# Kernel optimization log

Hardware: AMD Instinct MI355X
Metric: run time of the kernel (lower is better)

Reference implementation:

```python
import jax, jax.numpy as jnp
import numpy as np

N_NODES = 20000
NUM_STEPS = 6
SIGNS = (1.0, -1.0, 1.0, -1.0, 1.0, -1.0)  # TF_POS, TF_NEG, PPI_POS, PPI_NEG, UNDIR, MIRNA_NEG


def setup_inputs() -> dict:
    key = jax.random.key(0)
    ks = jax.random.split(key, 12)
    B, N, E, H, C = 64, N_NODES, 400000, 64, 32
    return {
        "ctl_base": jax.random.normal(ks[0], (B, N), jnp.float32),
        "u_raw": jax.random.normal(ks[1], (B, N), jnp.float32),
        "cell_idx": jax.random.randint(ks[2], (B,), 0, C, jnp.int32),
        "edge_src": jax.random.randint(ks[3], (6, E), 0, N, jnp.int32),
        "edge_dst": jax.random.randint(ks[4], (6, E), 0, N, jnp.int32),
        "edge_val": jax.random.uniform(ks[5], (6, E), jnp.float32),
        "g_logits": jnp.zeros((6,), jnp.float32),
        "alpha_logits": jnp.zeros((NUM_STEPS,), jnp.float32),
        "cell_emb": jax.random.normal(ks[6], (C, H), jnp.float32),
        "W1": jax.random.normal(ks[7], (3, H), jnp.float32) * 0.1,
        "b1": jnp.zeros((H,), jnp.float32),
        "W2": jax.random.normal(ks[8], (H, 1), jnp.float32) * 0.1,
        "b2": jnp.zeros((1,), jnp.float32),
    }


def _spmm_right(h, src, dst, val):
    # out[b, j] = sum_{e: dst[e]==j} h[b, src[e]] * val[e]   (== h @ A)
    gathered = h.T[src] * val[:, None]  # [E, B]
    return jax.ops.segment_sum(gathered, dst, num_segments=N_NODES).T  # [B, N]


def reference(ctl_base, u_raw, g_logits, alpha_logits, cell_emb,
              W1, b1, W2, b2, edge_val, edge_src, edge_dst, cell_idx):
    g = jax.nn.softplus(g_logits)          # [6] relation gates
    alphas = jax.nn.sigmoid(alpha_logits)  # [num_steps]
    h0 = u_raw
    h = u_raw
    for k in range(NUM_STEPS):
        msg = jnp.zeros_like(h)
        for r in range(6):
            msg = msg + SIGNS[r] * g[r] * _spmm_right(h, edge_src[r], edge_dst[r], edge_val[r])
        a = alphas[k]
        h = a * h0 + (1.0 - a) * msg
    # decode: stack [ctl, u_raw, hK] -> [B, N, 3]
    x = jnp.stack([ctl_base, u_raw, h], axis=-1)
    hd = jax.nn.relu(jnp.einsum('bnf,fh->bnh', x, W1) + b1)  # [B, N, H]
    hd = hd + cell_emb[cell_idx][:, None, :]
    y = (jnp.einsum('bnh,ho->bno', hd, W2) + b2)[..., 0]  # [B, N]
    return y
```

## Files before the change

### kernel.cpp

```cpp
#include <hip/hip_runtime.h>

#define N_NODES 20000
#define HID 64
#define NSTEPS 6
#define NSLICE 8
#define SLICE_SZ (N_NODES / NSLICE)
#define SUBB 64
#define NBLK (NSLICE * SUBB)
#define NB1 512
#define MAGIC 13422

union U16H { unsigned short u; _Float16 h; };
union U4H8 { uint4 u; _Float16 h[8]; };

__device__ __forceinline__ _Float16 us_as_h(unsigned short s) { U16H u; u.u = s; return u.h; }
__device__ __forceinline__ unsigned short h_as_us(_Float16 h) { U16H u; u.h = h; return u.u; }

__device__ __forceinline__ int slice_of(int d) {
    return (int)(((unsigned)d * (unsigned)MAGIC) >> 25);
}
__device__ __forceinline__ float softplusf_(float x) {
    return (x > 0.f) ? (x + log1pf(expf(-x))) : log1pf(expf(x));
}
__device__ __forceinline__ float sigmoidf_(float x) {
    return 1.f / (1.f + expf(-x));
}

__global__ __launch_bounds__(64) void prep_kernel(const float* __restrict__ g_logits,
                                                  const float* __restrict__ alpha_logits,
                                                  const int* __restrict__ cell_idx,
                                                  const float* __restrict__ cell_emb,
                                                  const float* __restrict__ W2,
                                                  const float* __restrict__ b2,
                                                  float* __restrict__ gsign,
                                                  float* __restrict__ alph,
                                                  float* __restrict__ cell_dot) {
    int t = threadIdx.x;
    if (t < 6) gsign[t] = ((t & 1) ? -1.f : 1.f) * softplusf_(g_logits[t]);
    if (t < NSTEPS) alph[t] = sigmoidf_(alpha_logits[t]);
    int ci = cell_idx[t];
    float acc = b2[0];
    for (int hh = 0; hh < HID; ++hh) acc = fmaf(cell_emb[ci * HID + hh], W2[hh], acc);
    cell_dot[t] = acc;
}

__global__ __launch_bounds__(256) void count8_kernel(const int* __restrict__ edst,
                                                     int* __restrict__ gcnt, int TE) {
    __shared__ int lh[8];
    int bk = blockIdx.x;
    int lane = threadIdx.x & 63;
    if (threadIdx.x < 8) lh[threadIdx.x] = 0;
    __syncthreads();
    int chunk = ((TE + NB1 - 1) / NB1 + 255) & ~255;
    int lo = bk * chunk;
    int hi = min(lo + chunk, TE);
    int my = 0;
    for (int ii = 0; ii < chunk; ii += 256) {
        int i = lo + ii + (int)threadIdx.x;
        bool act = i < hi;
        int s = -1;
        if (act) s = slice_of(__builtin_nontemporal_load(edst + i));
#pragma unroll
        for (int q = 0; q < 8; ++q) {
            unsigned long long b = __ballot(s == q);
            if (lane == q) my += (int)__popcll(b);
        }
    }
    if (lane < 8) atomicAdd(&lh[lane], my);
    __syncthreads();
    if (threadIdx.x < 8) gcnt[bk * 8 + threadIdx.x] = lh[threadIdx.x];
}

__global__ __launch_bounds__(256) void scan8_kernel(const int* __restrict__ gcnt,
                                                    int* __restrict__ blkoff,
                                                    int* __restrict__ bbase) {
    __shared__ int psum[8][33];
    int tid = threadIdx.x;
    int s = tid >> 5, g = tid & 31;
    const int per = NB1 / 32;
    int sum = 0;
    for (int b = g * per; b < (g + 1) * per; ++b) sum += gcnt[b * 8 + s];
    psum[s][g] = sum;
    __syncthreads();
    if (tid < 8) {
        int run = 0;
        for (int i = 0; i < 32; ++i) { int v = psum[tid][i]; psum[tid][i] = run; run += v; }
        psum[tid][32] = run;
    }
    __syncthreads();
    int run = psum[s][g];
    for (int b = g * per; b < (g + 1) * per; ++b) {
        blkoff[b * 8 + s] = run;
        run += gcnt[b * 8 + s];
    }
    if (tid == 0) {
        int acc = 0;
        bbase[0] = 0;
        for (int q = 0; q < 8; ++q) { acc += psum[q][32]; bbase[q + 1] = acc; }
    }
}

__global__ __launch_bounds__(256) void bucket_kernel(const int* __restrict__ esrc,
                                                     const int* __restrict__ edst,
                                                     const float* __restrict__ eval,
                                                     const float* __restrict__ gsign,
                                                     const int* __restrict__ blkoff,
                                                     const int* __restrict__ bbase,
                                                     int2* __restrict__ bucket,
                                                     int E, int TE) {
    __shared__ int lcur[8];
    int bk = blockIdx.x;
    int lane = threadIdx.x & 63;
    if (threadIdx.x < 8) lcur[threadIdx.x] = bbase[threadIdx.x] + blkoff[bk * 8 + threadIdx.x];
    __syncthreads();
    int chunk = ((TE + NB1 - 1) / NB1 + 255) & ~255;
    int lo = bk * chunk;
    int hi = min(lo + chunk, TE);
    for (int ii = 0; ii < chunk; ii += 256) {
        int i = lo + ii + (int)threadIdx.x;
        bool act = i < hi;
        int s = -1, meta = 0, cb = 0;
        if (act) {
            int d  = __builtin_nontemporal_load(edst + i);
            int sv = __builtin_nontemporal_load(esrc + i);
            float ev = __builtin_nontemporal_load(eval + i);
            s = slice_of(d);
            int dl = d - s * SLICE_SZ;
            meta = sv | (dl << 16);
            int r = (i >= E) + (i >= 2 * E) + (i >= 3 * E) + (i >= 4 * E) + (i >= 5 * E);
            cb = __float_as_int(gsign[r] * ev);
        }
        int pos = 0;
#pragma unroll
        for (int q = 0; q < 8; ++q) {
            unsigned long long b = __ballot(s == q);
            if (b) {
                int leader = (int)__ffsll(b) - 1;
                int base = 0;
                if (lane == leader) base = atomicAdd(&lcur[q], (int)__popcll(b));
                base = __shfl(base, leader);
                if (s == q) pos = base + (int)__popcll(b & ((1ull << lane) - 1ull));
            }
        }
        if (act) bucket[pos] = make_int2(meta, cb);
    }
}

__global__ __launch_bounds__(256) void hist2db_kernel(const int2* __restrict__ bucket,
                                                      const int* __restrict__ bbase,
                                                      int* __restrict__ blkcnt) {
    __shared__ int lh[SLICE_SZ];
    int bk = blockIdx.x;
    int slice = bk & (NSLICE - 1);
    int sub = bk >> 3;
    for (int b = threadIdx.x; b < SLICE_SZ; b += 256) lh[b] = 0;
    __syncthreads();
    int lo = bbase[slice];
    int total = bbase[slice + 1] - lo;
    int chunk = ((total + SUBB - 1) / SUBB + 255) & ~255;
    int beg = lo + sub * chunk;
    int end = min(beg + chunk, lo + total);
    const int* mp = (const int*)bucket;
    for (int i = beg + (int)threadIdx.x; i < end; i += 256) {
        int meta = __builtin_nontemporal_load(mp + 2 * (size_t)i);
        atomicAdd(&lh[((unsigned)meta) >> 16], 1);
    }
    __syncthreads();
    int* out = blkcnt + (size_t)(slice * SUBB + sub) * SLICE_SZ;
    for (int b = threadIdx.x; b < SLICE_SZ; b += 256) out[b] = lh[b];
}

__global__ __launch_bounds__(256) void colscan_kernel(int* __restrict__ blkcnt,
                                                      int* __restrict__ counts) {
    int n = blockIdx.x * 256 + threadIdx.x;
    if (n >= N_NODES) return;
    int slice = n / SLICE_SZ, bin = n % SLICE_SZ;
    size_t base = (size_t)slice * SUBB * SLICE_SZ + bin;
    int run = 0;
#pragma unroll 8
    for (int s = 0; s < SUBB; ++s) {
        size_t idx = base + (size_t)s * SLICE_SZ;
        int t = blkcnt[idx];
        blkcnt[idx] = run;
        run += t;
    }
    counts[n] = run;
}

__global__ __launch_bounds__(256) void scan_kernel(const int* __restrict__ counts,
                                                   int* __restrict__ grp_ptr, int n) {
    __shared__ int sums[256];
    int tid = threadIdx.x;
    int seg = (n + 255) >> 8;
    int beg = tid * seg;
    int end = min(beg + seg, n);
    int s = 0;
    for (int i = beg; i < end; ++i) s += (counts[i] + 7) >> 3;
    sums[tid] = s;
    __syncthreads();
    if (tid == 0) {
        int run = 0;
        for (int i = 0; i < 256; ++i) { int v = sums[i]; sums[i] = run; run += v; }
        grp_ptr[n] = run;
    }
    __syncthreads();
    int off = sums[tid];
    for (int i = beg; i < end; ++i) {
        grp_ptr[i] = off;
        off += (counts[i] + 7) >> 3;
    }
}

__global__ __launch_bounds__(256) void scatter2b_kernel(const int2* __restrict__ bucket,
                                                        const int* __restrict__ bbase,
                                                        const int* __restrict__ grp_ptr,
                                                        const int* __restrict__ blkcnt,
                                                        unsigned* __restrict__ eg) {
    __shared__ int lbase[SLICE_SZ];
    int bk = blockIdx.x;
    int slice = bk & (NSLICE - 1);
    int sub = bk >> 3;
    int lo_n = slice * SLICE_SZ;
    const int* boff = blkcnt + (size_t)(slice * SUBB + sub) * SLICE_SZ;
    for (int b = threadIdx.x; b < SLICE_SZ; b += 256)
        lbase[b] = grp_ptr[lo_n + b] * 8 + boff[b];
    __syncthreads();
    int lo = bbase[slice];
    int total = bbase[slice + 1] - lo;
    int chunk = ((total + SUBB - 1) / SUBB + 255) & ~255;
    int beg = lo + sub * chunk;
    int end = min(beg + chunk, lo + total);
    for (int i = beg + (int)threadIdx.x; i < end; i += 256) {
        long long rec = __builtin_nontemporal_load((const long long*)bucket + i);
        int meta = (int)rec;
        float cf = __int_as_float((int)(rec >> 32));
        int pos = atomicAdd(&lbase[((unsigned)meta) >> 16], 1);
        eg[pos] = (unsigned)(meta & 0xFFFF) | ((unsigned)h_as_us((_Float16)cf) << 16);
    }
}

__global__ __launch_bounds__(256) void transpose64(float* __restrict__ out,
                                                   _Float16* __restrict__ outh,
                                                   const float* __restrict__ in,
                                                   int R, int C) {
    __shared__ float tile[64][65];
    int c0 = blockIdx.x * 64, r0 = blockIdx.y * 64;
    int tx = threadIdx.x & 63, ty = threadIdx.x >> 6;
#pragma unroll
    for (int i = 0; i < 16; ++i) {
        int r = r0 + ty + i * 4;
        int c = c0 + tx;
        tile[ty + i * 4][tx] = (r < R && c < C) ? in[(size_t)r * C + c] : 0.f;
    }
    __syncthreads();
#pragma unroll
    for (int i = 0; i < 16; ++i) {
        int c = c0 + ty + i * 4;
        int r = r0 + tx;
        if (c < C && r < R) {
            float v = tile[tx][ty + i * 4];
            out[(size_t)c * R + r] = v;
            if (outh) outh[(size_t)c * R + r] = (_Float16)v;
        }
    }
}

__global__ __launch_bounds__(256) void step_kernel(const _Float16* __restrict__ h_in,
                                                   const float* __restrict__ h0,
                                                   _Float16* __restrict__ h_out,
                                                   float* __restrict__ hF,
                                                   const int* __restrict__ grp_ptr,
                                                   const unsigned* __restrict__ eg,
                                                   const float* __restrict__ alph,
                                                   int k, int last) {
    int lane = threadIdx.x & 63;
    int node = blockIdx.x * 4 + (threadIdx.x >> 6);
    if (node >= N_NODES) return;
    int gb = __builtin_amdgcn_readfirstlane(grp_ptr[node]);
    int ge = __builtin_amdgcn_readfirstlane(grp_ptr[node + 1]);
    int sub8 = lane >> 3;
    const _Float16* hbase = h_in + (lane & 7) * 8;
    float acc[8] = {0.f, 0.f, 0.f, 0.f, 0.f, 0.f, 0.f, 0.f};
    int g = gb;
    for (; g + 2 <= ge; g += 2) {
        unsigned e0 = eg[(size_t)g * 8 + sub8];
        unsigned e1 = eg[(size_t)(g + 1) * 8 + sub8];
        U4H8 v0, v1;
        v0.u = *(const uint4*)(hbase + (e0 & 0xFFFFu) * 64);
        v1.u = *(const uint4*)(hbase + (e1 & 0xFFFFu) * 64);
        float c0 = (float)us_as_h((unsigned short)(e0 >> 16));
        float c1 = (float)us_as_h((unsigned short)(e1 >> 16));
#pragma unroll
        for (int j = 0; j < 8; ++j) acc[j] = fmaf((float)v0.h[j], c0, acc[j]);
#pragma unroll
        for (int j = 0; j < 8; ++j) acc[j] = fmaf((float)v1.h[j], c1, acc[j]);
    }
    for (; g < ge; ++g) {
        unsigned e0 = eg[(size_t)g * 8 + sub8];
        U4H8 v0;
        v0.u = *(const uint4*)(hbase + (e0 & 0xFFFFu) * 64);
        float c0 = (float)us_as_h((unsigned short)(e0 >> 16));
#pragma unroll
        for (int j = 0; j < 8; ++j) acc[j] = fmaf((float)v0.h[j], c0, acc[j]);
    }
#pragma unroll
    for (int st = 8; st < 64; st <<= 1) {
#pragma unroll
        for (int j = 0; j < 8; ++j) acc[j] += __shfl_xor(acc[j], st, 64);
    }
    if (lane < 8) {
        float a = alph[k];
        int base = node * 64 + lane * 8;
        float4 h0a = *(const float4*)(h0 + base);
        float4 h0b = *(const float4*)(h0 + base + 4);
        float om = 1.f - a;
        float r0 = fmaf(a, h0a.x, om * acc[0]);
        float r1 = fmaf(a, h0a.y, om * acc[1]);
        float r2 = fmaf(a, h0a.z, om * acc[2]);
        float r3 = fmaf(a, h0a.w, om * acc[3]);
        float r4 = fmaf(a, h0b.x, om * acc[4]);
        float r5 = fmaf(a, h0b.y, om * acc[5]);
        float r6 = fmaf(a, h0b.z, om * acc[6]);
        float r7 = fmaf(a, h0b.w, om * acc[7]);
        if (last) {
            *(float4*)(hF + base)     = make_float4(r0, r1, r2, r3);
            *(float4*)(hF + base + 4) = make_float4(r4, r5, r6, r7);
        } else {
            U4H8 o;
            o.h[0] = (_Float16)r0; o.h[1] = (_Float16)r1;
            o.h[2] = (_Float16)r2; o.h[3] = (_Float16)r3;
            o.h[4] = (_Float16)r4; o.h[5] = (_Float16)r5;
            o.h[6] = (_Float16)r6; o.h[7] = (_Float16)r7;
            *(uint4*)(h_out + base) = o.u;
        }
    }
}

__global__ __launch_bounds__(256) void decode_kernel(float* __restrict__ y,
                                                     const float* __restrict__ ctl,
                                                     const float* __restrict__ u,
                                                     const float* __restrict__ h_bn,
                                                     const float* __restrict__ W1,
                                                     const float* __restrict__ b1,
                                                     const float* __restrict__ W2,
                                                     const float* __restrict__ cell_dot,
                                                     int total) {
    __shared__ float4 pack[HID];
    __shared__ float w2s[HID];
    if (threadIdx.x < HID) {
        int hh = threadIdx.x;
        pack[hh] = make_float4(W1[0 * HID + hh], W1[1 * HID + hh], W1[2 * HID + hh], b1[hh]);
        w2s[hh] = W2[hh];
    }
    __syncthreads();
    int idx = blockIdx.x * 256 + threadIdx.x;
    if (idx >= total) return;
    int b = idx / N_NODES;
    float xc = ctl[idx], xu = u[idx], xh = h_bn[idx];
    float acc = 0.f;
#pragma unroll 8
    for (int hh = 0; hh < HID; ++hh) {
        float4 p = pack[hh];
        float t = fmaf(xc, p.x, fmaf(xu, p.y, fmaf(xh, p.z, p.w)));
        t = fmaxf(t, 0.f);
        acc = fmaf(t, w2s[hh], acc);
    }
    y[idx] = acc + cell_dot[b];
}

extern "C" void kernel_launch(void* const* d_in, const int* in_sizes, int n_in,
                              void* d_out, int out_size, void* d_ws, size_t ws_size,
                              hipStream_t stream) {
    const float* ctl          = (const float*)d_in[0];
    const float* u_raw        = (const float*)d_in[1];
    const int*   cell_idx     = (const int*)d_in[2];
    const int*   edge_src     = (const int*)d_in[3];
    const int*   edge_dst     = (const int*)d_in[4];
    const float* edge_val     = (const float*)d_in[5];
    const float* g_logits     = (const float*)d_in[6];
    const float* alpha_logits = (const float*)d_in[7];
    const float* cell_emb     = (const float*)d_in[8];
    const float* W1           = (const float*)d_in[9];
    const float* b1           = (const float*)d_in[10];
    const float* W2           = (const float*)d_in[11];
    const float* b2           = (const float*)d_in[12];
    float* y = (float*)d_out;

    const int TE = in_sizes[3];
    const int E  = TE / 6;
    const int NB = N_NODES * 64;

    char* ws = (char*)d_ws;
    size_t off = 0;
    auto alloc = [&](size_t bytes) -> char* {
        char* p = ws + off;
        off += (bytes + 255) & ~(size_t)255;
        return p;
    };
    int* grp_ptr = (int*)alloc((N_NODES + 1) * sizeof(int));
    int* counts  = (int*)alloc(N_NODES * sizeof(int));
    int* blkcnt  = (int*)alloc((size_t)NSLICE * SUBB * SLICE_SZ * sizeof(int));
    int* gcnt    = (int*)alloc((size_t)NB1 * 8 * sizeof(int));
    int* blkoff  = (int*)alloc((size_t)NB1 * 8 * sizeof(int));
    int* bbase   = (int*)alloc(16 * sizeof(int));
    const size_t MAXG = (size_t)TE / 8 + N_NODES + 8;
    unsigned* eg = (unsigned*)alloc(MAXG * 8 * sizeof(unsigned));
    size_t need_h = (size_t)NB * (2 + 2 + 2 + 4 + 4);
    size_t ov_sz = (size_t)TE * sizeof(int2);
    if (ov_sz < need_h) ov_sz = need_h;
    char* overlay = alloc(ov_sz);
    float* u_t      = (float*)alloc((size_t)NB * sizeof(float));
    float* gsign    = (float*)alloc(8 * sizeof(float));
    float* alph     = (float*)alloc(8 * sizeof(float));
    float* cell_dot = (float*)alloc(64 * sizeof(float));

    int2* bucket = (int2*)overlay;
    _Float16* uh  = (_Float16*)overlay;
    _Float16* hA  = (_Float16*)(overlay + (size_t)NB * 2);
    _Float16* hB  = (_Float16*)(overlay + (size_t)NB * 4);
    float* hF   = (float*)(overlay + (size_t)NB * 6);
    float* h_bn = (float*)(overlay + (size_t)NB * 10);

    prep_kernel<<<1, 64, 0, stream>>>(g_logits, alpha_logits, cell_idx, cell_emb,
                                      W2, b2, gsign, alph, cell_dot);
    hipMemsetAsync(eg, 0, MAXG * 8 * sizeof(unsigned), stream);

    count8_kernel<<<NB1, 256, 0, stream>>>(edge_dst, gcnt, TE);
    scan8_kernel<<<1, 256, 0, stream>>>(gcnt, blkoff, bbase);
    bucket_kernel<<<NB1, 256, 0, stream>>>(edge_src, edge_dst, edge_val, gsign,
                                           blkoff, bbase, bucket, E, TE);
    hist2db_kernel<<<NBLK, 256, 0, stream>>>(bucket, bbase, blkcnt);
    colscan_kernel<<<(N_NODES + 255) / 256, 256, 0, stream>>>(blkcnt, counts);
    scan_kernel<<<1, 256, 0, stream>>>(counts, grp_ptr, N_NODES);
    scatter2b_kernel<<<NBLK, 256, 0, stream>>>(bucket, bbase, grp_ptr, blkcnt, eg);

    transpose64<<<dim3((N_NODES + 63) / 64, 1), 256, 0, stream>>>(u_t, uh, u_raw,
                                                                  64, N_NODES);

    const _Float16* hin = uh;
    for (int k = 0; k < NSTEPS; ++k) {
        _Float16* hout = (k & 1) ? hB : hA;
        step_kernel<<<(N_NODES + 3) / 4, 256, 0, stream>>>(hin, u_t, hout, hF, grp_ptr,
                                                           eg, alph, k, k == NSTEPS - 1);
        hin = hout;
    }

    transpose64<<<dim3(1, (N_NODES + 63) / 64), 256, 0, stream>>>(h_bn, (_Float16*)0,
                                                                  hF, N_NODES, 64);

    decode_kernel<<<(out_size + 255) / 256, 256, 0, stream>>>(y, ctl, u_raw, h_bn,
                                                              W1, b1, W2, cell_dot, out_size);
}
```

Baseline: 398.4 us.

## Fuse small preprocessing kernels, transposes and memset into neighbouring kernels

Folds the prep kernel into scan8, the eg memset into count8, the u_raw transpose into extra blocks of scatter2b, and the final h transpose into decode via an in-block tile. The single-block scan is rewritten as a wave-shuffle scan. The overlay aliasing is replaced with separate buffers, which is needed now that the transpose runs alongside the scatter while bucket is still live. The aim is fewer launches and one fewer global round trip of h, at the cost of more workspace and heavier blocks.

```diff
diff --git a/kernel.cpp b/kernel.cpp
--- a/kernel.cpp
+++ b/kernel.cpp
@@ -7,9 +7,13 @@
 #define SLICE_SZ (N_NODES / NSLICE)
 #define SUBB 64
 #define NBLK (NSLICE * SUBB)
+#define TBLK ((N_NODES + 63) / 64)
 #define NB1 512
 #define MAGIC 13422
 
+typedef _Float16 h8_t __attribute__((ext_vector_type(8)));
+typedef unsigned u4_t __attribute__((ext_vector_type(4)));
+
 union U16H { unsigned short u; _Float16 h; };
 union U4H8 { uint4 u; _Float16 h[8]; };
 
@@ -26,26 +30,14 @@
     return 1.f / (1.f + expf(-x));
 }
 
-__global__ __launch_bounds__(64) void prep_kernel(const float* __restrict__ g_logits,
-                                                  const float* __restrict__ alpha_logits,
-                                                  const int* __restrict__ cell_idx,
-                                                  const float* __restrict__ cell_emb,
-                                                  const float* __restrict__ W2,
-                                                  const float* __restrict__ b2,
-                                                  float* __restrict__ gsign,
-                                                  float* __restrict__ alph,
-                                                  float* __restrict__ cell_dot) {
-    int t = threadIdx.x;
-    if (t < 6) gsign[t] = ((t & 1) ? -1.f : 1.f) * softplusf_(g_logits[t]);
-    if (t < NSTEPS) alph[t] = sigmoidf_(alpha_logits[t]);
-    int ci = cell_idx[t];
-    float acc = b2[0];
-    for (int hh = 0; hh < HID; ++hh) acc = fmaf(cell_emb[ci * HID + hh], W2[hh], acc);
-    cell_dot[t] = acc;
-}
-
 __global__ __launch_bounds__(256) void count8_kernel(const int* __restrict__ edst,
-                                                     int* __restrict__ gcnt, int TE) {
+                                                     int* __restrict__ gcnt, int TE,
+                                                     u4_t* __restrict__ egq, long long egq_n) {
+    u4_t z = {0u, 0u, 0u, 0u};
+    for (long long i = (long long)blockIdx.x * 256 + threadIdx.x; i < egq_n;
+         i += (long long)NB1 * 256)
+        __builtin_nontemporal_store(z, egq + i);
+
     __shared__ int lh[8];
     int bk = blockIdx.x;
     int lane = threadIdx.x & 63;
@@ -73,7 +65,16 @@
 
 __global__ __launch_bounds__(256) void scan8_kernel(const int* __restrict__ gcnt,
                                                     int* __restrict__ blkoff,
-                                                    int* __restrict__ bbase) {
+                                                    int* __restrict__ bbase,
+                                                    const float* __restrict__ g_logits,
+                                                    const float* __restrict__ alpha_logits,
+                                                    const int* __restrict__ cell_idx,
+                                                    const float* __restrict__ cell_emb,
+                                                    const float* __restrict__ W2,
+                                                    const float* __restrict__ b2,
+                                                    float* __restrict__ gsign,
+                                                    float* __restrict__ alph,
+                                                    float* __restrict__ cell_dot) {
     __shared__ int psum[8][33];
     int tid = threadIdx.x;
     int s = tid >> 5, g = tid & 31;
@@ -97,6 +98,14 @@
         int acc = 0;
         bbase[0] = 0;
         for (int q = 0; q < 8; ++q) { acc += psum[q][32]; bbase[q + 1] = acc; }
+    }
+    if (tid < 64) {
+        if (tid < 6) gsign[tid] = ((tid & 1) ? -1.f : 1.f) * softplusf_(g_logits[tid]);
+        if (tid < NSTEPS) alph[tid] = sigmoidf_(alpha_logits[tid]);
+        int ci = cell_idx[tid];
+        float acc = b2[0];
+        for (int hh = 0; hh < HID; ++hh) acc = fmaf(cell_emb[ci * HID + hh], W2[hh], acc);
+        cell_dot[tid] = acc;
     }
 }
 
@@ -189,35 +198,65 @@
 
 __global__ __launch_bounds__(256) void scan_kernel(const int* __restrict__ counts,
                                                    int* __restrict__ grp_ptr, int n) {
-    __shared__ int sums[256];
+    __shared__ int wsum[4];
     int tid = threadIdx.x;
-    int seg = (n + 255) >> 8;
-    int beg = tid * seg;
-    int end = min(beg + seg, n);
-    int s = 0;
-    for (int i = beg; i < end; ++i) s += (counts[i] + 7) >> 3;
-    sums[tid] = s;
-    __syncthreads();
-    if (tid == 0) {
-        int run = 0;
-        for (int i = 0; i < 256; ++i) { int v = sums[i]; sums[i] = run; run += v; }
-        grp_ptr[n] = run;
-    }
-    __syncthreads();
-    int off = sums[tid];
-    for (int i = beg; i < end; ++i) {
-        grp_ptr[i] = off;
-        off += (counts[i] + 7) >> 3;
-    }
+    int lane = tid & 63, wid = tid >> 6;
+    int carry = 0;
+    for (int base = 0; base < n; base += 256) {
+        int i = base + tid;
+        int v = (i < n) ? ((counts[i] + 7) >> 3) : 0;
+        int x = v;
+#pragma unroll
+        for (int st = 1; st < 64; st <<= 1) {
+            int t = __shfl_up(x, st, 64);
+            if (lane >= st) x += t;
+        }
+        if (lane == 63) wsum[wid] = x;
+        __syncthreads();
+        int w0 = wsum[0], w1 = wsum[1], w2 = wsum[2], w3 = wsum[3];
+        int woff = carry;
+        if (wid > 0) woff += w0;
+        if (wid > 1) woff += w1;
+        if (wid > 2) woff += w2;
+        if (i < n) grp_ptr[i] = woff + x - v;
+        carry += w0 + w1 + w2 + w3;
+        __syncthreads();
+    }
+    if (tid == 0) grp_ptr[n] = carry;
 }
 
 __global__ __launch_bounds__(256) void scatter2b_kernel(const int2* __restrict__ bucket,
                                                         const int* __restrict__ bbase,
                                                         const int* __restrict__ grp_ptr,
                                                         const int* __restrict__ blkcnt,
-                                                        unsigned* __restrict__ eg) {
-    __shared__ int lbase[SLICE_SZ];
+                                                        unsigned* __restrict__ eg,
+                                                        const float* __restrict__ u_raw,
+                                                        float* __restrict__ u_t,
+                                                        _Float16* __restrict__ uh) {
+    __shared__ float smem[64 * 65];
     int bk = blockIdx.x;
+    if (bk >= NBLK) {
+        float(*tile)[65] = (float(*)[65])smem;
+        int c0 = (bk - NBLK) * 64;
+        int tx = threadIdx.x & 63, ty = threadIdx.x >> 6;
+#pragma unroll
+        for (int i = 0; i < 16; ++i) {
+            int c = c0 + tx;
+            tile[ty + i * 4][tx] = (c < N_NODES) ? u_raw[(size_t)(ty + i * 4) * N_NODES + c] : 0.f;
+        }
+        __syncthreads();
+#pragma unroll
+        for (int i = 0; i < 16; ++i) {
+            int c = c0 + ty + i * 4;
+            if (c < N_NODES) {
+                float v = tile[tx][ty + i * 4];
+                u_t[(size_t)c * 64 + tx] = v;
+                uh[(size_t)c * 64 + tx] = (_Float16)v;
+            }
+        }
+        return;
+    }
+    int* lbase = (int*)smem;
     int slice = bk & (NSLICE - 1);
     int sub = bk >> 3;
     int lo_n = slice * SLICE_SZ;
@@ -236,32 +275,6 @@
         float cf = __int_as_float((int)(rec >> 32));
         int pos = atomicAdd(&lbase[((unsigned)meta) >> 16], 1);
         eg[pos] = (unsigned)(meta & 0xFFFF) | ((unsigned)h_as_us((_Float16)cf) << 16);
-    }
-}
-
-__global__ __launch_bounds__(256) void transpose64(float* __restrict__ out,
-                                                   _Float16* __restrict__ outh,
-                                                   const float* __restrict__ in,
-                                                   int R, int C) {
-    __shared__ float tile[64][65];
-    int c0 = blockIdx.x * 64, r0 = blockIdx.y * 64;
-    int tx = threadIdx.x & 63, ty = threadIdx.x >> 6;
-#pragma unroll
-    for (int i = 0; i < 16; ++i) {
-        int r = r0 + ty + i * 4;
-        int c = c0 + tx;
-        tile[ty + i * 4][tx] = (r < R && c < C) ? in[(size_t)r * C + c] : 0.f;
-    }
-    __syncthreads();
-#pragma unroll
-    for (int i = 0; i < 16; ++i) {
-        int c = c0 + ty + i * 4;
-        int r = r0 + tx;
-        if (c < C && r < R) {
-            float v = tile[tx][ty + i * 4];
-            out[(size_t)c * R + r] = v;
-            if (outh) outh[(size_t)c * R + r] = (_Float16)v;
-        }
     }
 }
 
@@ -284,24 +297,22 @@
     int g = gb;
     for (; g + 2 <= ge; g += 2) {
         unsigned e0 = eg[(size_t)g * 8 + sub8];
-        unsigned e1 = eg[(size_t)(g + 1) * 8 + sub8];
-        U4H8 v0, v1;
-        v0.u = *(const uint4*)(hbase + (e0 & 0xFFFFu) * 64);
-        v1.u = *(const uint4*)(hbase + (e1 & 0xFFFFu) * 64);
+        unsigned e1 = eg[(size_t)g * 8 + 8 + sub8];
+        h8_t v0 = *(const h8_t*)(hbase + (e0 & 0xFFFFu) * 64);
+        h8_t v1 = *(const h8_t*)(hbase + (e1 & 0xFFFFu) * 64);
         float c0 = (float)us_as_h((unsigned short)(e0 >> 16));
         float c1 = (float)us_as_h((unsigned short)(e1 >> 16));
 #pragma unroll
-        for (int j = 0; j < 8; ++j) acc[j] = fmaf((float)v0.h[j], c0, acc[j]);
-#pragma unroll
-        for (int j = 0; j < 8; ++j) acc[j] = fmaf((float)v1.h[j], c1, acc[j]);
-    }
-    for (; g < ge; ++g) {
+        for (int j = 0; j < 8; ++j) acc[j] = fmaf((float)v0[j], c0, acc[j]);
+#pragma unroll
+        for (int j = 0; j < 8; ++j) acc[j] = fmaf((float)v1[j], c1, acc[j]);
+    }
+    if (g < ge) {
         unsigned e0 = eg[(size_t)g * 8 + sub8];
-        U4H8 v0;
-        v0.u = *(const uint4*)(hbase + (e0 & 0xFFFFu) * 64);
+        h8_t v0 = *(const h8_t*)(hbase + (e0 & 0xFFFFu) * 64);
         float c0 = (float)us_as_h((unsigned short)(e0 >> 16));
 #pragma unroll
-        for (int j = 0; j < 8; ++j) acc[j] = fmaf((float)v0.h[j], c0, acc[j]);
+        for (int j = 0; j < 8; ++j) acc[j] = fmaf((float)v0[j], c0, acc[j]);
     }
 #pragma unroll
     for (int st = 8; st < 64; st <<= 1) {
@@ -339,33 +350,47 @@
 __global__ __launch_bounds__(256) void decode_kernel(float* __restrict__ y,
                                                      const float* __restrict__ ctl,
                                                      const float* __restrict__ u,
-                                                     const float* __restrict__ h_bn,
+                                                     const float* __restrict__ hF,
                                                      const float* __restrict__ W1,
                                                      const float* __restrict__ b1,
                                                      const float* __restrict__ W2,
-                                                     const float* __restrict__ cell_dot,
-                                                     int total) {
+                                                     const float* __restrict__ cell_dot) {
+    __shared__ float tile[64][65];
     __shared__ float4 pack[HID];
     __shared__ float w2s[HID];
+    __shared__ float cds[64];
     if (threadIdx.x < HID) {
         int hh = threadIdx.x;
         pack[hh] = make_float4(W1[0 * HID + hh], W1[1 * HID + hh], W1[2 * HID + hh], b1[hh]);
         w2s[hh] = W2[hh];
-    }
-    __syncthreads();
-    int idx = blockIdx.x * 256 + threadIdx.x;
-    if (idx >= total) return;
-    int b = idx / N_NODES;
-    float xc = ctl[idx], xu = u[idx], xh = h_bn[idx];
-    float acc = 0.f;
+        cds[hh] = cell_dot[hh];
+    }
+    int n0 = blockIdx.x * 64;
+    int tx = threadIdx.x & 63, ty = threadIdx.x >> 6;
+#pragma unroll
+    for (int i = 0; i < 16; ++i) {
+        int n = n0 + ty + i * 4;
+        tile[ty + i * 4][tx] = (n < N_NODES) ? hF[(size_t)n * 64 + tx] : 0.f;
+    }
+    __syncthreads();
+#pragma unroll
+    for (int i = 0; i < 16; ++i) {
+        int b = ty + i * 4;
+        int n = n0 + tx;
+        if (n < N_NODES) {
+            size_t idx = (size_t)b * N_NODES + n;
+            float xc = ctl[idx], xu = u[idx], xh = tile[tx][b];
+            float acc = 0.f;
 #pragma unroll 8
-    for (int hh = 0; hh < HID; ++hh) {
-        float4 p = pack[hh];
-        float t = fmaf(xc, p.x, fmaf(xu, p.y, fmaf(xh, p.z, p.w)));
-        t = fmaxf(t, 0.f);
-        acc = fmaf(t, w2s[hh], acc);
-    }
-    y[idx] = acc + cell_dot[b];
+            for (int hh = 0; hh < HID; ++hh) {
+                float4 p = pack[hh];
+                float t = fmaf(xc, p.x, fmaf(xu, p.y, fmaf(xh, p.z, p.w)));
+                t = fmaxf(t, 0.f);
+                acc = fmaf(t, w2s[hh], acc);
+            }
+            y[idx] = acc + cds[b];
+        }
+    }
 }
 
 extern "C" void kernel_launch(void* const* d_in, const int* in_sizes, int n_in,
@@ -405,37 +430,28 @@
     int* bbase   = (int*)alloc(16 * sizeof(int));
     const size_t MAXG = (size_t)TE / 8 + N_NODES + 8;
     unsigned* eg = (unsigned*)alloc(MAXG * 8 * sizeof(unsigned));
-    size_t need_h = (size_t)NB * (2 + 2 + 2 + 4 + 4);
-    size_t ov_sz = (size_t)TE * sizeof(int2);
-    if (ov_sz < need_h) ov_sz = need_h;
-    char* overlay = alloc(ov_sz);
+    int2* bucket    = (int2*)alloc((size_t)TE * sizeof(int2));
+    _Float16* uh    = (_Float16*)alloc((size_t)NB * 2);
+    _Float16* hA    = (_Float16*)alloc((size_t)NB * 2);
+    _Float16* hB    = (_Float16*)alloc((size_t)NB * 2);
+    float* hF       = (float*)alloc((size_t)NB * 4);
     float* u_t      = (float*)alloc((size_t)NB * sizeof(float));
     float* gsign    = (float*)alloc(8 * sizeof(float));
     float* alph     = (float*)alloc(8 * sizeof(float));
     float* cell_dot = (float*)alloc(64 * sizeof(float));
 
-    int2* bucket = (int2*)overlay;
-    _Float16* uh  = (_Float16*)overlay;
-    _Float16* hA  = (_Float16*)(overlay + (size_t)NB * 2);
-    _Float16* hB  = (_Float16*)(overlay + (size_t)NB * 4);
-    float* hF   = (float*)(overlay + (size_t)NB * 6);
-    float* h_bn = (float*)(overlay + (size_t)NB * 10);
-
-    prep_kernel<<<1, 64, 0, stream>>>(g_logits, alpha_logits, cell_idx, cell_emb,
-                                      W2, b2, gsign, alph, cell_dot);
-    hipMemsetAsync(eg, 0, MAXG * 8 * sizeof(unsigned), stream);
-
-    count8_kernel<<<NB1, 256, 0, stream>>>(edge_dst, gcnt, TE);
-    scan8_kernel<<<1, 256, 0, stream>>>(gcnt, blkoff, bbase);
+    count8_kernel<<<NB1, 256, 0, stream>>>(edge_dst, gcnt, TE,
+                                           (u4_t*)eg, (long long)(MAXG * 2));
+    scan8_kernel<<<1, 256, 0, stream>>>(gcnt, blkoff, bbase, g_logits, alpha_logits,
+                                        cell_idx, cell_emb, W2, b2,
+                                        gsign, alph, cell_dot);
     bucket_kernel<<<NB1, 256, 0, stream>>>(edge_src, edge_dst, edge_val, gsign,
                                            blkoff, bbase, bucket, E, TE);
     hist2db_kernel<<<NBLK, 256, 0, stream>>>(bucket, bbase, blkcnt);
     colscan_kernel<<<(N_NODES + 255) / 256, 256, 0, stream>>>(blkcnt, counts);
     scan_kernel<<<1, 256, 0, stream>>>(counts, grp_ptr, N_NODES);
-    scatter2b_kernel<<<NBLK, 256, 0, stream>>>(bucket, bbase, grp_ptr, blkcnt, eg);
-
-    transpose64<<<dim3((N_NODES + 63) / 64, 1), 256, 0, stream>>>(u_t, uh, u_raw,
-                                                                  64, N_NODES);
+    scatter2b_kernel<<<NBLK + TBLK, 256, 0, stream>>>(bucket, bbase, grp_ptr, blkcnt,
+                                                      eg, u_raw, u_t, uh);
 
     const _Float16* hin = uh;
     for (int k = 0; k < NSTEPS; ++k) {
@@ -445,9 +461,5 @@
         hin = hout;
     }
 
-    transpose64<<<dim3(1, (N_NODES + 63) / 64), 256, 0, stream>>>(h_bn, (_Float16*)0,
-                                                                  hF, N_NODES, 64);
-
-    decode_kernel<<<(out_size + 255) / 256, 256, 0, stream>>>(y, ctl, u_raw, h_bn,
-                                                              W1, b1, W2, cell_dot, out_size);
-}
+    decode_kernel<<<TBLK, 256, 0, stream>>>(y, ctl, u_raw, hF, W1, b1, W2, cell_dot);
+}
```

Result: slower. 410.0 us (+2.9%).
